# Kernel optimization log

Hardware: AMD Instinct MI355X
Metric: run time of the kernel (lower is better)

The kernel has to match this reference:

```python
import jax, jax.numpy as jnp
import numpy as np

EMBED_DIM = 1024
NUM_HEADS = 16
HEAD_DIM = EMBED_DIM // NUM_HEADS
B, S = 2, 2048


def setup_inputs() -> dict:
    key = jax.random.key(0)
    ks = jax.random.split(key, 9)
    s = 1.0 / np.sqrt(EMBED_DIM)
    return {
        "x": jax.random.normal(ks[0], (B, S, EMBED_DIM), dtype=jnp.float32),
        "Wq": jax.random.normal(ks[1], (EMBED_DIM, EMBED_DIM), dtype=jnp.float32) * s,
        "bq": jnp.zeros((EMBED_DIM,), dtype=jnp.float32),
        "Wk": jax.random.normal(ks[2], (EMBED_DIM, EMBED_DIM), dtype=jnp.float32) * s,
        "bk": jnp.zeros((EMBED_DIM,), dtype=jnp.float32),
        "Wv": jax.random.normal(ks[3], (EMBED_DIM, EMBED_DIM), dtype=jnp.float32) * s,
        "bv": jnp.zeros((EMBED_DIM,), dtype=jnp.float32),
        "Wo": jax.random.normal(ks[4], (EMBED_DIM, EMBED_DIM), dtype=jnp.float32) * s,
        "bo": jnp.zeros((EMBED_DIM,), dtype=jnp.float32),
    }


def reference(x, Wq, bq, Wk, bk, Wv, bv, Wo, bo):
    b, s, _ = x.shape
    # Projections; reshape to [B, H, S, Dh]
    def proj(W, bias):
        return (x @ W + bias).reshape(b, s, NUM_HEADS, HEAD_DIM).transpose(0, 2, 1, 3)
    q = proj(Wq, bq)
    k = proj(Wk, bk)
    v = proj(Wv, bv)
    scale = 1.0 / np.sqrt(HEAD_DIM).astype(np.float32)
    scores = jnp.einsum('bhqd,bhkd->bhqk', q, k) * scale  # [B,H,S,S]
    attn = jax.nn.softmax(scores, axis=-1)
    out = jnp.einsum('bhqk,bhkd->bhqd', attn, v)  # [B,H,S,Dh]
    out = out.transpose(0, 2, 1, 3).reshape(b, s, EMBED_DIM)
    return out @ Wo + bo
```

## Files before the change

kernel.cpp:

```cpp
#include <hip/hip_runtime.h>
#include <hip/hip_bf16.h>

typedef unsigned short ushort_t;
typedef __attribute__((ext_vector_type(8))) short short8;
typedef __attribute__((ext_vector_type(4))) float f32x4;
typedef __attribute__((ext_vector_type(16))) float f32x16;
typedef __attribute__((ext_vector_type(2))) unsigned int uint2v;

#define EMBED 1024
#define NHEAD 16
#define HDIM 64
#define BB 2
#define SSEQ 2048
#define MROWS (BB*SSEQ)
#define QKV_N (3*EMBED)
#define PER_BUF (MROWS*EMBED)

__device__ __forceinline__ ushort_t f2bf(float f) {
    union { float f; unsigned int u; } x; x.f = f;
    unsigned int r = x.u + 0x7fffu + ((x.u >> 16) & 1u);
    return (ushort_t)(r >> 16);
}
__device__ __forceinline__ unsigned pack2bf(float lo, float hi) {
    return (unsigned)f2bf(lo) | ((unsigned)f2bf(hi) << 16);
}

__device__ __forceinline__ void gload16(const void* g, void* l) {
    __builtin_amdgcn_global_load_lds(
        (const __attribute__((address_space(1))) unsigned int*)g,
        (__attribute__((address_space(3))) unsigned int*)l, 16, 0, 0);
}

__global__ void cast_bf16_kernel(const float* __restrict__ in, ushort_t* __restrict__ out, int n) {
    int i = (blockIdx.x * blockDim.x + threadIdx.x) * 4;
    if (i + 3 < n) {
        float4 v = *(const float4*)(in + i);
        out[i+0] = f2bf(v.x); out[i+1] = f2bf(v.y);
        out[i+2] = f2bf(v.z); out[i+3] = f2bf(v.w);
    }
}

__global__ void transpose_cast_kernel(const float* __restrict__ W, ushort_t* __restrict__ Wt) {
    __shared__ float tile[32][33];
    int tx = threadIdx.x, ty = threadIdx.y;
    int n0 = blockIdx.x * 32, k0 = blockIdx.y * 32;
    #pragma unroll
    for (int i = 0; i < 4; i++)
        tile[ty*4+i][tx] = W[(size_t)(k0 + ty*4 + i) * EMBED + n0 + tx];
    __syncthreads();
    #pragma unroll
    for (int i = 0; i < 4; i++)
        Wt[(size_t)(n0 + ty*4 + i) * EMBED + k0 + tx] = f2bf(tile[tx][ty*4+i]);
}

__global__ void transpose_v_kernel(const ushort_t* __restrict__ v, ushort_t* __restrict__ vt) {
    __shared__ ushort_t tile[64][66];
    int bh = blockIdx.y, s0 = blockIdx.x * 64;
    int t = threadIdx.x;
    int r = t >> 3, c8 = (t & 7) * 8;
    #pragma unroll
    for (int p = 0; p < 2; p++) {
        short8 vv = *(const short8*)&v[((size_t)bh*SSEQ + s0 + p*32 + r)*HDIM + c8];
        #pragma unroll
        for (int j = 0; j < 8; j++) tile[p*32 + r][c8 + j] = (ushort_t)vv[j];
    }
    __syncthreads();
    #pragma unroll
    for (int p = 0; p < 2; p++) {
        int d = p*32 + r;
        short8 ov;
        #pragma unroll
        for (int j = 0; j < 8; j++) ov[j] = (short)tile[c8 + j][d];
        *(short8*)&vt[((size_t)bh*HDIM + d)*SSEQ + s0 + c8] = ov;
    }
}

template<int OUT_MODE>
__global__ __launch_bounds__(256) void gemm_bt_kernel(
    const ushort_t* __restrict__ A,
    const ushort_t* __restrict__ Bt,
    const float* __restrict__ b0, const float* __restrict__ b1, const float* __restrict__ b2,
    void* __restrict__ Cout,
    int M, int N, int K)
{
    __shared__ __attribute__((aligned(16))) ushort_t Asm[128*32];
    __shared__ __attribute__((aligned(16))) ushort_t Bsm[128*32];
    int t = threadIdx.x;
    int w = t >> 6, l = t & 63;
    int wr = w >> 1, wc = w & 1;
    int lrow = l & 15, lhi = l >> 4;
    int m0 = blockIdx.y * 128, n0 = blockIdx.x * 128;
    int srow = l >> 2;
    int scol = (l & 3) * 8;

    f32x4 acc[4][4];
    #pragma unroll
    for (int mi = 0; mi < 4; mi++)
        #pragma unroll
        for (int ni = 0; ni < 4; ni++)
            #pragma unroll
            for (int c = 0; c < 4; c++) acc[mi][ni][c] = 0.f;

    for (int k0 = 0; k0 < K; k0 += 32) {
        __syncthreads();
        #pragma unroll
        for (int p = 0; p < 2; p++) {
            gload16(&A [(size_t)(m0 + w*32 + p*16 + srow)*K + k0 + scol], &Asm[(w*32 + p*16)*32]);
            gload16(&Bt[(size_t)(n0 + w*32 + p*16 + srow)*K + k0 + scol], &Bsm[(w*32 + p*16)*32]);
        }
        __syncthreads();
        short8 af[4], bfr[4];
        #pragma unroll
        for (int mi = 0; mi < 4; mi++)
            af[mi] = *(short8*)&Asm[(wr*64 + mi*16 + lrow)*32 + lhi*8];
        #pragma unroll
        for (int ni = 0; ni < 4; ni++)
            bfr[ni] = *(short8*)&Bsm[(wc*64 + ni*16 + lrow)*32 + lhi*8];
        #pragma unroll
        for (int mi = 0; mi < 4; mi++)
            #pragma unroll
            for (int ni = 0; ni < 4; ni++)
                acc[mi][ni] = __builtin_amdgcn_mfma_f32_16x16x32_bf16(af[mi], bfr[ni], acc[mi][ni], 0, 0, 0);
    }

    #pragma unroll
    for (int mi = 0; mi < 4; mi++)
        #pragma unroll
        for (int ni = 0; ni < 4; ni++) {
            int col = n0 + wc*64 + ni*16 + lrow;
            #pragma unroll
            for (int c = 0; c < 4; c++) {
                int row = m0 + wr*64 + mi*16 + lhi*4 + c;
                if (OUT_MODE == 0) {
                    float v = acc[mi][ni][c] + b0[col];
                    ((float*)Cout)[(size_t)row * N + col] = v;
                } else {
                    int which = col >> 10, hc = col & 1023;
                    const float* bp = (which == 0) ? b0 : (which == 1) ? b1 : b2;
                    float v = acc[mi][ni][c] + bp[hc];
                    if (which == 0) v *= 0.18033688011112042f;
                    int h = hc >> 6, d = hc & 63;
                    int b = row >> 11, s = row & 2047;
                    ((ushort_t*)Cout)[(size_t)which*PER_BUF + ((size_t)((b*NHEAD + h)*SSEQ) + s)*HDIM + d] = f2bf(v);
                }
            }
        }
}

#define MFMA32(a,b,c) __builtin_amdgcn_mfma_f32_32x32x16_bf16(a, b, c, 0, 0, 0)

__global__ __launch_bounds__(256, 2) void flash_attn2_kernel(
    const ushort_t* __restrict__ q,
    const ushort_t* __restrict__ k,
    const ushort_t* __restrict__ vt,
    ushort_t* __restrict__ o)
{
    __shared__ __attribute__((aligned(16))) ushort_t Ks[2][64*64];
    __shared__ __attribute__((aligned(16))) ushort_t Vs[2][64*64];

    int t = threadIdx.x, w = t >> 6, l = t & 63;
    int l31 = l & 31, hi = l >> 5;

    int flat = blockIdx.x;
    int wg = (flat & 7) * 64 + (flat >> 3);
    int bh = wg >> 4;
    int q0 = (wg & 15) * 128;

    const ushort_t* qp = q  + (size_t)bh * SSEQ * HDIM;
    const ushort_t* kp = k  + (size_t)bh * SSEQ * HDIM;
    const ushort_t* vp = vt + (size_t)bh * HDIM * SSEQ;

    int lr = l >> 3, lc = l & 7;
    int colel = 8 * (lc ^ lr);

    short8 qf[4];
    int qrow = q0 + w*32 + l31;
    #pragma unroll
    for (int st = 0; st < 4; st++)
        qf[st] = *(const short8*)&qp[(size_t)qrow*HDIM + st*16 + hi*8];

    f32x16 o0 = {}, o1 = {};
    float m_run = -1e30f, l_run = 0.f;

    #define STAGE(buf, kv0) { \
        _Pragma("unroll") \
        for (int c = 0; c < 2; c++) { \
            int row = w*16 + c*8 + lr; \
            gload16(&kp[(size_t)(kv0 + row)*HDIM + colel], &Ks[buf][(w*16 + c*8)*64]); \
            gload16(&vp[(size_t)row*SSEQ + (kv0) + colel], &Vs[buf][(w*16 + c*8)*64]); \
        } }

    STAGE(0, 0)
    asm volatile("s_waitcnt vmcnt(0)");
    __syncthreads();
    int cur = 0;

    for (int kv0 = 0; kv0 < SSEQ; kv0 += 64) {
        if (kv0 + 64 < SSEQ) { STAGE(cur ^ 1, kv0 + 64) }

        f32x16 s0 = {}, s1 = {};
        #pragma unroll
        for (int st = 0; st < 4; st++) {
            int colb = st*16 + hi*8;
            short8 kf0 = *(const short8*)&Ks[cur][l31*64        + (colb ^ ((l31 & 7) << 3))];
            short8 kf1 = *(const short8*)&Ks[cur][(32 + l31)*64 + (colb ^ ((l31 & 7) << 3))];
            s0 = MFMA32(kf0, qf[st], s0);
            s1 = MFMA32(kf1, qf[st], s1);
        }

        float mx = s0[0];
        #pragma unroll
        for (int r = 1; r < 16; r++) mx = fmaxf(mx, s0[r]);
        #pragma unroll
        for (int r = 0; r < 16; r++) mx = fmaxf(mx, s1[r]);
        mx = fmaxf(mx, __shfl_xor(mx, 32));

        if (__any(mx > m_run + 8.f)) {
            float mnew = fmaxf(m_run, mx);
            float alpha = __builtin_amdgcn_exp2f(m_run - mnew);
            #pragma unroll
            for (int r = 0; r < 16; r++) { o0[r] *= alpha; o1[r] *= alpha; }
            l_run *= alpha;
            m_run = mnew;
        }
        float rs = 0.f;
        #pragma unroll
        for (int r = 0; r < 16; r++) { s0[r] = __builtin_amdgcn_exp2f(s0[r] - m_run); rs += s0[r]; }
        #pragma unroll
        for (int r = 0; r < 16; r++) { s1[r] = __builtin_amdgcn_exp2f(s1[r] - m_run); rs += s1[r]; }
        rs += __shfl_xor(rs, 32);
        l_run += rs;

        short8 pfr[4];
        #pragma unroll
        for (int kt = 0; kt < 2; kt++) {
            #pragma unroll
            for (int sub = 0; sub < 2; sub++) {
                float e0, e1, e2, e3, e4, e5, e6, e7;
                if (kt == 0 && sub == 0) { e0=s0[0];e1=s0[1];e2=s0[2];e3=s0[3];e4=s0[4];e5=s0[5];e6=s0[6];e7=s0[7]; }
                else if (kt == 0)        { e0=s0[8];e1=s0[9];e2=s0[10];e3=s0[11];e4=s0[12];e5=s0[13];e6=s0[14];e7=s0[15]; }
                else if (sub == 0)       { e0=s1[0];e1=s1[1];e2=s1[2];e3=s1[3];e4=s1[4];e5=s1[5];e6=s1[6];e7=s1[7]; }
                else                     { e0=s1[8];e1=s1[9];e2=s1[10];e3=s1[11];e4=s1[12];e5=s1[13];e6=s1[14];e7=s1[15]; }
                unsigned a0 = pack2bf(e0, e1);
                unsigned a1 = pack2bf(e2, e3);
                unsigned b0 = pack2bf(e4, e5);
                unsigned b1 = pack2bf(e6, e7);
                uint2v r0 = __builtin_amdgcn_permlane32_swap(a0, b0, false, false);
                uint2v r1 = __builtin_amdgcn_permlane32_swap(a1, b1, false, false);
                union { unsigned u[4]; short8 v; } pf;
                pf.u[0] = r0.x; pf.u[1] = r1.x; pf.u[2] = r0.y; pf.u[3] = r1.y;
                pfr[kt*2 + sub] = pf.v;
            }
        }

        #pragma unroll
        for (int ks = 0; ks < 4; ks++) {
            int colb = ks*16 + hi*8;
            short8 vf0 = *(const short8*)&Vs[cur][l31*64        + (colb ^ ((l31 & 7) << 3))];
            short8 vf1 = *(const short8*)&Vs[cur][(32 + l31)*64 + (colb ^ ((l31 & 7) << 3))];
            o0 = MFMA32(vf0, pfr[ks], o0);
            o1 = MFMA32(vf1, pfr[ks], o1);
        }

        asm volatile("s_waitcnt vmcnt(0)");
        __syncthreads();
        cur ^= 1;
    }

    float rl = 1.f / l_run;
    ushort_t* Ot = ((ushort_t*)Ks) + w*(32*64);
    #pragma unroll
    for (int dt = 0; dt < 2; dt++)
        #pragma unroll
        for (int rq = 0; rq < 4; rq++) {
            float v0 = (dt ? o1[rq*4+0] : o0[rq*4+0]) * rl;
            float v1 = (dt ? o1[rq*4+1] : o0[rq*4+1]) * rl;
            float v2 = (dt ? o1[rq*4+2] : o0[rq*4+2]) * rl;
            float v3 = (dt ? o1[rq*4+3] : o0[rq*4+3]) * rl;
            int d0 = dt*32 + rq*8 + hi*4;
            uint2v pw = { pack2bf(v0, v1), pack2bf(v2, v3) };
            *(uint2v*)&Ot[l31*64 + (d0 ^ ((l31 & 7) << 3))] = pw;
        }

    int b = bh >> 4, h = bh & 15;
    int q2 = l >> 1, dh = (l & 1) * 32;
    size_t obase = ((size_t)(b*SSEQ) + q0 + w*32 + q2)*EMBED + h*HDIM;
    #pragma unroll
    for (int j = 0; j < 4; j++) {
        int d = dh + j*8;
        short8 ov = *(short8*)&Ot[q2*64 + (d ^ ((q2 & 7) << 3))];
        *(short8*)&o[obase + d] = ov;
    }
}

extern "C" void kernel_launch(void* const* d_in, const int* in_sizes, int n_in,
                              void* d_out, int out_size, void* d_ws, size_t ws_size,
                              hipStream_t stream) {
    const float* x  = (const float*)d_in[0];
    const float* Wq = (const float*)d_in[1];
    const float* bq = (const float*)d_in[2];
    const float* Wk = (const float*)d_in[3];
    const float* bk = (const float*)d_in[4];
    const float* Wv = (const float*)d_in[5];
    const float* bv = (const float*)d_in[6];
    const float* Wo = (const float*)d_in[7];
    const float* bo = (const float*)d_in[8];

    char* ws = (char*)d_ws;
    ushort_t* xb  = (ushort_t*)(ws);
    ushort_t* WqT = (ushort_t*)(ws + (8u  << 20));
    ushort_t* WkT = (ushort_t*)(ws + (10u << 20));
    ushort_t* WvT = (ushort_t*)(ws + (12u << 20));
    ushort_t* WoT = (ushort_t*)(ws + (14u << 20));
    ushort_t* qb  = (ushort_t*)(ws + (16u << 20));
    ushort_t* kb  = (ushort_t*)(ws + (24u << 20));
    ushort_t* vb  = (ushort_t*)(ws + (32u << 20));
    ushort_t* vtb = (ushort_t*)(ws + (40u << 20));
    ushort_t* ab  = xb;

    int nx = MROWS * EMBED;
    cast_bf16_kernel<<<nx/(256*4), 256, 0, stream>>>(x, xb, nx);

    dim3 tb(32, 8), tg(EMBED/32, EMBED/32);
    transpose_cast_kernel<<<tg, tb, 0, stream>>>(Wq, WqT);
    transpose_cast_kernel<<<tg, tb, 0, stream>>>(Wk, WkT);
    transpose_cast_kernel<<<tg, tb, 0, stream>>>(Wv, WvT);
    transpose_cast_kernel<<<tg, tb, 0, stream>>>(Wo, WoT);

    gemm_bt_kernel<2><<<dim3(QKV_N/128, MROWS/128), 256, 0, stream>>>(
        xb, WqT, bq, bk, bv, qb, MROWS, QKV_N, EMBED);

    transpose_v_kernel<<<dim3(SSEQ/64, BB*NHEAD), 256, 0, stream>>>(vb, vtb);

    flash_attn2_kernel<<<512, 256, 0, stream>>>(qb, kb, vtb, ab);

    gemm_bt_kernel<0><<<dim3(EMBED/128, MROWS/128), 256, 0, stream>>>(
        ab, WoT, bo, bo, bo, d_out, MROWS, EMBED, EMBED);
}
```

Measured before the change: 146.0 us.

## Batch weight transposes, remap GEMM blocks across XCDs, raise MFMA priority, tune softmax

Merges the four weight transpose-cast launches into one launch with a z dimension. Remaps GEMM block indices so consecutive blocks spread across the 8 XCDs. Wraps MFMA sections in s_setprio to favour matrix issue. Splits the flash-attention max and sum reductions into independent chains for more ILP, and replaces software bf16 packing with the hardware v_cvt_pk_bf16_f32 instruction. Rounding of the packed conversion may differ slightly from the manual round-to-nearest-even code.

Result: faster. 132.8 us (-9.1%).

```diff
diff --git a/kernel.cpp b/kernel.cpp
--- a/kernel.cpp
+++ b/kernel.cpp
@@ -21,8 +21,10 @@
     unsigned int r = x.u + 0x7fffu + ((x.u >> 16) & 1u);
     return (ushort_t)(r >> 16);
 }
-__device__ __forceinline__ unsigned pack2bf(float lo, float hi) {
-    return (unsigned)f2bf(lo) | ((unsigned)f2bf(hi) << 16);
+__device__ __forceinline__ unsigned cvt_pk_bf16(float lo, float hi) {
+    unsigned r;
+    asm("v_cvt_pk_bf16_f32 %0, %1, %2" : "=v"(r) : "v"(lo), "v"(hi));
+    return r;
 }
 
 __device__ __forceinline__ void gload16(const void* g, void* l) {
@@ -40,8 +42,16 @@
     }
 }
 
-__global__ void transpose_cast_kernel(const float* __restrict__ W, ushort_t* __restrict__ Wt) {
+__global__ void transpose_cast4_kernel(
+    const float* __restrict__ W0, const float* __restrict__ W1,
+    const float* __restrict__ W2, const float* __restrict__ W3,
+    ushort_t* __restrict__ T0, ushort_t* __restrict__ T1,
+    ushort_t* __restrict__ T2, ushort_t* __restrict__ T3)
+{
     __shared__ float tile[32][33];
+    int z = blockIdx.z;
+    const float* W = (z == 0) ? W0 : (z == 1) ? W1 : (z == 2) ? W2 : W3;
+    ushort_t* Wt   = (z == 0) ? T0 : (z == 1) ? T1 : (z == 2) ? T2 : T3;
     int tx = threadIdx.x, ty = threadIdx.y;
     int n0 = blockIdx.x * 32, k0 = blockIdx.y * 32;
     #pragma unroll
@@ -89,7 +99,13 @@
     int w = t >> 6, l = t & 63;
     int wr = w >> 1, wc = w & 1;
     int lrow = l & 15, lhi = l >> 4;
-    int m0 = blockIdx.y * 128, n0 = blockIdx.x * 128;
+
+    int gx = gridDim.x;
+    int flat = blockIdx.y * gx + blockIdx.x;
+    int q8 = (gx * gridDim.y) >> 3;
+    int nf = (flat & 7) * q8 + (flat >> 3);
+    int m0 = (nf / gx) * 128, n0 = (nf % gx) * 128;
+
     int srow = l >> 2;
     int scol = (l & 3) * 8;
 
@@ -116,11 +132,13 @@
         #pragma unroll
         for (int ni = 0; ni < 4; ni++)
             bfr[ni] = *(short8*)&Bsm[(wc*64 + ni*16 + lrow)*32 + lhi*8];
+        __builtin_amdgcn_s_setprio(1);
         #pragma unroll
         for (int mi = 0; mi < 4; mi++)
             #pragma unroll
             for (int ni = 0; ni < 4; ni++)
                 acc[mi][ni] = __builtin_amdgcn_mfma_f32_16x16x32_bf16(af[mi], bfr[ni], acc[mi][ni], 0, 0, 0);
+        __builtin_amdgcn_s_setprio(0);
     }
 
     #pragma unroll
@@ -199,6 +217,7 @@
         if (kv0 + 64 < SSEQ) { STAGE(cur ^ 1, kv0 + 64) }
 
         f32x16 s0 = {}, s1 = {};
+        __builtin_amdgcn_s_setprio(1);
         #pragma unroll
         for (int st = 0; st < 4; st++) {
             int colb = st*16 + hi*8;
@@ -207,12 +226,25 @@
             s0 = MFMA32(kf0, qf[st], s0);
             s1 = MFMA32(kf1, qf[st], s1);
         }
-
-        float mx = s0[0];
-        #pragma unroll
-        for (int r = 1; r < 16; r++) mx = fmaxf(mx, s0[r]);
-        #pragma unroll
-        for (int r = 0; r < 16; r++) mx = fmaxf(mx, s1[r]);
+        __builtin_amdgcn_s_setprio(0);
+
+        float ma = fmaxf(s0[0], s0[1]);
+        float mb = fmaxf(s0[2], s0[3]);
+        float mc = fmaxf(s0[4], s0[5]);
+        float md = fmaxf(s0[6], s0[7]);
+        ma = fmaxf(fmaxf(ma, s0[8]),  s0[9]);
+        mb = fmaxf(fmaxf(mb, s0[10]), s0[11]);
+        mc = fmaxf(fmaxf(mc, s0[12]), s0[13]);
+        md = fmaxf(fmaxf(md, s0[14]), s0[15]);
+        ma = fmaxf(fmaxf(ma, s1[0]),  s1[1]);
+        mb = fmaxf(fmaxf(mb, s1[2]),  s1[3]);
+        mc = fmaxf(fmaxf(mc, s1[4]),  s1[5]);
+        md = fmaxf(fmaxf(md, s1[6]),  s1[7]);
+        ma = fmaxf(fmaxf(ma, s1[8]),  s1[9]);
+        mb = fmaxf(fmaxf(mb, s1[10]), s1[11]);
+        mc = fmaxf(fmaxf(mc, s1[12]), s1[13]);
+        md = fmaxf(fmaxf(md, s1[14]), s1[15]);
+        float mx = fmaxf(fmaxf(ma, mb), fmaxf(mc, md));
         mx = fmaxf(mx, __shfl_xor(mx, 32));
 
         if (__any(mx > m_run + 8.f)) {
@@ -223,11 +255,22 @@
             l_run *= alpha;
             m_run = mnew;
         }
-        float rs = 0.f;
-        #pragma unroll
-        for (int r = 0; r < 16; r++) { s0[r] = __builtin_amdgcn_exp2f(s0[r] - m_run); rs += s0[r]; }
-        #pragma unroll
-        for (int r = 0; r < 16; r++) { s1[r] = __builtin_amdgcn_exp2f(s1[r] - m_run); rs += s1[r]; }
+        float r0 = 0.f, r1 = 0.f, r2 = 0.f, r3 = 0.f;
+        #pragma unroll
+        for (int r = 0; r < 16; r += 4) {
+            s0[r]   = __builtin_amdgcn_exp2f(s0[r]   - m_run); r0 += s0[r];
+            s0[r+1] = __builtin_amdgcn_exp2f(s0[r+1] - m_run); r1 += s0[r+1];
+            s0[r+2] = __builtin_amdgcn_exp2f(s0[r+2] - m_run); r2 += s0[r+2];
+            s0[r+3] = __builtin_amdgcn_exp2f(s0[r+3] - m_run); r3 += s0[r+3];
+        }
+        #pragma unroll
+        for (int r = 0; r < 16; r += 4) {
+            s1[r]   = __builtin_amdgcn_exp2f(s1[r]   - m_run); r0 += s1[r];
+            s1[r+1] = __builtin_amdgcn_exp2f(s1[r+1] - m_run); r1 += s1[r+1];
+            s1[r+2] = __builtin_amdgcn_exp2f(s1[r+2] - m_run); r2 += s1[r+2];
+            s1[r+3] = __builtin_amdgcn_exp2f(s1[r+3] - m_run); r3 += s1[r+3];
+        }
+        float rs = (r0 + r1) + (r2 + r3);
         rs += __shfl_xor(rs, 32);
         l_run += rs;
 
@@ -236,23 +279,21 @@
         for (int kt = 0; kt < 2; kt++) {
             #pragma unroll
             for (int sub = 0; sub < 2; sub++) {
-                float e0, e1, e2, e3, e4, e5, e6, e7;
-                if (kt == 0 && sub == 0) { e0=s0[0];e1=s0[1];e2=s0[2];e3=s0[3];e4=s0[4];e5=s0[5];e6=s0[6];e7=s0[7]; }
-                else if (kt == 0)        { e0=s0[8];e1=s0[9];e2=s0[10];e3=s0[11];e4=s0[12];e5=s0[13];e6=s0[14];e7=s0[15]; }
-                else if (sub == 0)       { e0=s1[0];e1=s1[1];e2=s1[2];e3=s1[3];e4=s1[4];e5=s1[5];e6=s1[6];e7=s1[7]; }
-                else                     { e0=s1[8];e1=s1[9];e2=s1[10];e3=s1[11];e4=s1[12];e5=s1[13];e6=s1[14];e7=s1[15]; }
-                unsigned a0 = pack2bf(e0, e1);
-                unsigned a1 = pack2bf(e2, e3);
-                unsigned b0 = pack2bf(e4, e5);
-                unsigned b1 = pack2bf(e6, e7);
-                uint2v r0 = __builtin_amdgcn_permlane32_swap(a0, b0, false, false);
-                uint2v r1 = __builtin_amdgcn_permlane32_swap(a1, b1, false, false);
+                const f32x16& sv = (kt == 0) ? s0 : s1;
+                int b8 = sub * 8;
+                unsigned a0 = cvt_pk_bf16(sv[b8+0], sv[b8+1]);
+                unsigned a1 = cvt_pk_bf16(sv[b8+2], sv[b8+3]);
+                unsigned b0 = cvt_pk_bf16(sv[b8+4], sv[b8+5]);
+                unsigned b1 = cvt_pk_bf16(sv[b8+6], sv[b8+7]);
+                uint2v rr0 = __builtin_amdgcn_permlane32_swap(a0, b0, false, false);
+                uint2v rr1 = __builtin_amdgcn_permlane32_swap(a1, b1, false, false);
                 union { unsigned u[4]; short8 v; } pf;
-                pf.u[0] = r0.x; pf.u[1] = r1.x; pf.u[2] = r0.y; pf.u[3] = r1.y;
+                pf.u[0] = rr0.x; pf.u[1] = rr1.x; pf.u[2] = rr0.y; pf.u[3] = rr1.y;
                 pfr[kt*2 + sub] = pf.v;
             }
         }
 
+        __builtin_amdgcn_s_setprio(1);
         #pragma unroll
         for (int ks = 0; ks < 4; ks++) {
             int colb = ks*16 + hi*8;
@@ -261,6 +302,7 @@
             o0 = MFMA32(vf0, pfr[ks], o0);
             o1 = MFMA32(vf1, pfr[ks], o1);
         }
+        __builtin_amdgcn_s_setprio(0);
 
         asm volatile("s_waitcnt vmcnt(0)");
         __syncthreads();
@@ -278,7 +320,7 @@
             float v2 = (dt ? o1[rq*4+2] : o0[rq*4+2]) * rl;
             float v3 = (dt ? o1[rq*4+3] : o0[rq*4+3]) * rl;
             int d0 = dt*32 + rq*8 + hi*4;
-            uint2v pw = { pack2bf(v0, v1), pack2bf(v2, v3) };
+            uint2v pw = { cvt_pk_bf16(v0, v1), cvt_pk_bf16(v2, v3) };
             *(uint2v*)&Ot[l31*64 + (d0 ^ ((l31 & 7) << 3))] = pw;
         }
 
@@ -321,11 +363,8 @@
     int nx = MROWS * EMBED;
     cast_bf16_kernel<<<nx/(256*4), 256, 0, stream>>>(x, xb, nx);
 
-    dim3 tb(32, 8), tg(EMBED/32, EMBED/32);
-    transpose_cast_kernel<<<tg, tb, 0, stream>>>(Wq, WqT);
-    transpose_cast_kernel<<<tg, tb, 0, stream>>>(Wk, WkT);
-    transpose_cast_kernel<<<tg, tb, 0, stream>>>(Wv, WvT);
-    transpose_cast_kernel<<<tg, tb, 0, stream>>>(Wo, WoT);
+    transpose_cast4_kernel<<<dim3(EMBED/32, EMBED/32, 4), dim3(32, 8), 0, stream>>>(
+        Wq, Wk, Wv, Wo, WqT, WkT, WvT, WoT);
 
     gemm_bt_kernel<2><<<dim3(QKV_N/128, MROWS/128), 256, 0, stream>>>(
         xb, WqT, bq, bk, bv, qb, MROWS, QKV_N, EMBED);
```
